# Kernel optimization log

Measured on AMD Instinct MI355X. Metric: run time of the kernel, lower is better.

Reference implementation:

```python
import jax, jax.numpy as jnp
import numpy as np

D_MODEL = 1280
NUM_EXPERTS = 20
HEAD_DIM = D_MODEL // NUM_EXPERTS  # 64
SCALE = HEAD_DIM ** -0.5


def setup_inputs() -> dict:
    key = jax.random.key(0)
    ks = jax.random.split(key, 8)
    B, S = 4, 1024
    s_in = 1.0 / np.sqrt(D_MODEL)
    x = jax.random.normal(ks[0], (B, S, D_MODEL), dtype=jnp.float32)
    # per-expert QKV projections stacked: [E, d_model, 3*head_dim]
    wqkv = jax.random.uniform(ks[1], (NUM_EXPERTS, D_MODEL, 3 * HEAD_DIM), jnp.float32, -s_in, s_in)
    bqkv = jax.random.uniform(ks[2], (NUM_EXPERTS, 3 * HEAD_DIM), jnp.float32, -s_in, s_in)
    router_w = jax.random.uniform(ks[3], (D_MODEL, NUM_EXPERTS), jnp.float32, -s_in, s_in)
    router_b = jax.random.uniform(ks[4], (NUM_EXPERTS,), jnp.float32, -s_in, s_in)
    out_w = jax.random.uniform(ks[5], (D_MODEL, D_MODEL), jnp.float32, -s_in, s_in)
    out_b = jax.random.uniform(ks[6], (D_MODEL,), jnp.float32, -s_in, s_in)
    return {"x": x, "wqkv": wqkv, "bqkv": bqkv, "router_w": router_w,
            "router_b": router_b, "out_w": out_w, "out_b": out_b}


def reference(x, wqkv, bqkv, router_w, router_b, out_w, out_b):
    # x: [B, S, D]
    B, S, D = x.shape
    E, H = NUM_EXPERTS, HEAD_DIM
    # router softmax gates (dropout = identity in eval)
    gates = jax.nn.softmax(x @ router_w + router_b, axis=-1)  # [B, S, E]
    # per-expert QKV: [E, B, S, 3H]
    qkv = jnp.einsum('bsd,edh->ebsh', x, wqkv) + bqkv[:, None, None, :]
    q, k, v = jnp.split(qkv, 3, axis=-1)  # each [E, B, S, H]
    scores = jnp.einsum('ebqh,ebkh->ebqk', q, k) * SCALE  # [E, B, S, S]
    attn = jax.nn.softmax(scores, axis=-1)
    eo = jnp.einsum('ebqk,ebkh->ebqh', attn, v)  # [E, B, S, H]
    # gate multiply and scatter into disjoint feature slices == concat over experts
    eo = eo * jnp.transpose(gates, (2, 0, 1))[..., None]  # [E, B, S, H]
    combined = jnp.transpose(eo, (1, 2, 0, 3)).reshape(B, S, E * H)  # [B, S, D]
    return combined @ out_w + out_b
```

## Files before the change

### kernel.cpp

```cpp
#include <hip/hip_runtime.h>
#include <hip/hip_bf16.h>

#define D_MODEL 1280
#define NUM_EXPERTS 20
#define HEAD_DIM 64
#define SEQ 1024
#define BATCH 4
#define BS_TOK 4096
#define QKV_N 192
#define QKV_W 3840

typedef __attribute__((ext_vector_type(8))) short short8;
typedef __attribute__((ext_vector_type(4))) float f32x4;
typedef __attribute__((ext_vector_type(16))) float f32x16;
typedef __hip_bfloat16 bf16;

static __device__ __forceinline__ void gload_lds16(const void* g, void* l) {
  __builtin_amdgcn_global_load_lds((const __attribute__((address_space(1))) void*)g,
                                   (__attribute__((address_space(3))) void*)l, 16, 0, 0);
}

__global__ __launch_bounds__(256) void k_rwT(const float* __restrict__ in,
                                             float* __restrict__ out) {
  int i = blockIdx.x * 256 + threadIdx.x;
  if (i < D_MODEL * NUM_EXPERTS) {
    int d = i / NUM_EXPERTS, e = i % NUM_EXPERTS;
    out[e * D_MODEL + d] = in[i];
  }
}

__global__ __launch_bounds__(256) void k_gates(const float* __restrict__ x,
    const float* __restrict__ rwT, const float* __restrict__ rb,
    float* __restrict__ gates, bf16* __restrict__ xb)
{
  __shared__ float xs[4][D_MODEL];
  __shared__ float logits[4][NUM_EXPERTS];
  const int r0 = blockIdx.x * 4;
  for (int i = threadIdx.x; i < 4 * (D_MODEL / 2); i += 256) {
    int r = i / (D_MODEL / 2), d2 = (i % (D_MODEL / 2)) * 2;
    float2 v = *(const float2*)(x + (size_t)(r0 + r) * D_MODEL + d2);
    xs[r][d2] = v.x; xs[r][d2 + 1] = v.y;
    __hip_bfloat162 h;
    h.x = __float2bfloat16(v.x); h.y = __float2bfloat16(v.y);
    *(__hip_bfloat162*)(xb + (size_t)(r0 + r) * D_MODEL + d2) = h;
  }
  __syncthreads();
  const int wid = threadIdx.x >> 6, lane = threadIdx.x & 63;
  for (int e = 0; e < NUM_EXPERTS; ++e) {
    float s = 0.f;
    #pragma unroll
    for (int j = 0; j < D_MODEL / 64; ++j) {
      int d = lane + 64 * j;
      s += xs[wid][d] * rwT[e * D_MODEL + d];
    }
    #pragma unroll
    for (int m = 32; m >= 1; m >>= 1) s += __shfl_xor(s, m);
    if (lane == 0) logits[wid][e] = s + rb[e];
  }
  __syncthreads();
  if (lane < 32) {
    float v = (lane < NUM_EXPERTS) ? logits[wid][lane] : -1e30f;
    float mx = v;
    #pragma unroll
    for (int m = 16; m >= 1; m >>= 1) mx = fmaxf(mx, __shfl_xor(mx, m, 32));
    float p = (lane < NUM_EXPERTS) ? __expf(v - mx) : 0.f;
    float sum = p;
    #pragma unroll
    for (int m = 16; m >= 1; m >>= 1) sum += __shfl_xor(sum, m, 32);
    if (lane < NUM_EXPERTS)
      gates[(size_t)(r0 + wid) * NUM_EXPERTS + lane] = p / sum;
  }
}

__global__ __launch_bounds__(256) void k_transpose(const float* __restrict__ in,
    bf16* __restrict__ out, int R, int C)
{
  __shared__ float tile[32][33];
  const size_t bo = (size_t)blockIdx.z * R * C;
  const int c0 = blockIdx.x * 32, r0 = blockIdx.y * 32;
  const int tx = threadIdx.x, ty = threadIdx.y;
  #pragma unroll
  for (int i = 0; i < 4; ++i)
    tile[ty + 8*i][tx] = in[bo + (size_t)(r0 + ty + 8*i) * C + (c0 + tx)];
  __syncthreads();
  #pragma unroll
  for (int i = 0; i < 4; ++i)
    out[bo + (size_t)(c0 + ty + 8*i) * R + (r0 + tx)] =
        __float2bfloat16(tile[tx][ty + 8*i]);
}

__global__ __launch_bounds__(512, 2) void k_gemm256(
    const bf16* __restrict__ A, const bf16* __restrict__ BT,
    const float* __restrict__ bias, bf16* __restrict__ C,
    int M, int N, int K)
{
  __shared__ __align__(16) bf16 lds[4][2][256 * 32];
  const int bid = blockIdx.x;
  const int xcd = bid & 7, c = bid >> 3;
  const int m0 = (xcd * 2 + (c & 1)) * 256;
  const int n0 = (c >> 1) * 256;
  const int tid = threadIdx.x, wid = tid >> 6, lane = tid & 63;
  const int wr = wid >> 2, wcn = wid & 3;
  const int fr = lane & 15, fg = lane >> 4;
  const int nt = K / 32;

  auto STAGE = [&](int t, int buf) {
    const bf16* Ag = A + (size_t)m0 * K + t * 32;
    const bf16* Bg = BT + (size_t)n0 * K + t * 32;
    #pragma unroll
    for (int i = 0; i < 2; ++i) {
      int idx = i * 512 + tid;
      int row = idx >> 2, sc = idx & 3;
      int g = sc ^ (row & 3);
      gload_lds16(Ag + (size_t)row * K + g * 8, &lds[buf][0][idx * 8]);
    }
    #pragma unroll
    for (int i = 0; i < 2; ++i) {
      int idx = i * 512 + tid;
      int row = idx >> 2, sc = idx & 3;
      int g = sc ^ (row & 3);
      gload_lds16(Bg + (size_t)row * K + g * 8, &lds[buf][1][idx * 8]);
    }
  };

  f32x4 acc[8][4] = {};
  auto COMPUTE = [&](int buf) {
    const bf16* As_ = &lds[buf][0][0];
    const bf16* Bs_ = &lds[buf][1][0];
    short8 af[8], bfv[4];
    #pragma unroll
    for (int mi = 0; mi < 8; ++mi) {
      int row = wr * 128 + mi * 16 + fr;
      int slot = fg ^ (row & 3);
      af[mi] = *(const short8*)(As_ + row * 32 + slot * 8);
    }
    #pragma unroll
    for (int ni = 0; ni < 4; ++ni) {
      int row = wcn * 64 + ni * 16 + fr;
      int slot = fg ^ (row & 3);
      bfv[ni] = *(const short8*)(Bs_ + row * 32 + slot * 8);
    }
    __builtin_amdgcn_s_setprio(1);
    #pragma unroll
    for (int mi = 0; mi < 8; ++mi) {
      #pragma unroll
      for (int ni = 0; ni < 4; ++ni)
        acc[mi][ni] = __builtin_amdgcn_mfma_f32_16x16x32_bf16(
            af[mi], bfv[ni], acc[mi][ni], 0, 0, 0);
    }
    __builtin_amdgcn_s_setprio(0);
  };

  STAGE(0, 0); STAGE(1, 1); STAGE(2, 2);
  asm volatile("s_waitcnt vmcnt(8)" ::: "memory");
  __builtin_amdgcn_s_barrier();
  __builtin_amdgcn_sched_barrier(0);
  int buf = 0;
  for (int t = 0; t < nt - 3; ++t) {
    int nb = buf + 3; nb = (nb >= 4) ? nb - 4 : nb;
    STAGE(t + 3, nb);
    COMPUTE(buf);
    asm volatile("s_waitcnt vmcnt(8)" ::: "memory");
    __builtin_amdgcn_s_barrier();
    __builtin_amdgcn_sched_barrier(0);
    buf = (buf == 3) ? 0 : buf + 1;
  }
  COMPUTE(buf);
  asm volatile("s_waitcnt vmcnt(4)" ::: "memory");
  __builtin_amdgcn_s_barrier();
  __builtin_amdgcn_sched_barrier(0);
  buf = (buf == 3) ? 0 : buf + 1;
  COMPUTE(buf);
  asm volatile("s_waitcnt vmcnt(0)" ::: "memory");
  __builtin_amdgcn_s_barrier();
  __builtin_amdgcn_sched_barrier(0);
  buf = (buf == 3) ? 0 : buf + 1;
  COMPUTE(buf);

  #pragma unroll
  for (int mi = 0; mi < 8; ++mi) {
    const int gr = m0 + wr * 128 + mi * 16 + fg * 4;
    #pragma unroll
    for (int ni = 0; ni < 4; ++ni) {
      const int gc = n0 + wcn * 64 + ni * 16 + fr;
      const float bv = bias[gc];
      #pragma unroll
      for (int r = 0; r < 4; ++r)
        C[(size_t)(gr + r) * N + gc] = __float2bfloat16(acc[mi][ni][r] + bv);
    }
  }
}

__global__ __launch_bounds__(512, 2) void k_gemm128r(
    const bf16* __restrict__ A, const bf16* __restrict__ BT,
    const float* __restrict__ bias, float* __restrict__ C,
    int M, int N, int K)
{
  __shared__ __align__(16) bf16 lds[4][2][128 * 32];
  const int bid = blockIdx.x;
  const int xcd = bid & 7, c = bid >> 3;
  const int m0 = (xcd * 4 + (c & 3)) * 128;
  const int n0 = (c >> 2) * 128;
  const int tid = threadIdx.x, wid = tid >> 6, lane = tid & 63;
  const int wr = wid >> 2, wcn = wid & 3;
  const int fr = lane & 15, fg = lane >> 4;
  const int nt = K / 32;

  auto STAGE = [&](int t, int buf) {
    const bf16* Ag = A + (size_t)m0 * K + t * 32;
    const bf16* Bg = BT + (size_t)n0 * K + t * 32;
    int row = tid >> 2, sc = tid & 3;
    int g = sc ^ (row & 3);
    gload_lds16(Ag + (size_t)row * K + g * 8, &lds[buf][0][tid * 8]);
    gload_lds16(Bg + (size_t)row * K + g * 8, &lds[buf][1][tid * 8]);
  };

  f32x4 acc[4][2] = {};
  auto COMPUTE = [&](int buf) {
    const bf16* As_ = &lds[buf][0][0];
    const bf16* Bs_ = &lds[buf][1][0];
    short8 af[4], bfv[2];
    #pragma unroll
    for (int mi = 0; mi < 4; ++mi) {
      int row = wr * 64 + mi * 16 + fr;
      int slot = fg ^ (row & 3);
      af[mi] = *(const short8*)(As_ + row * 32 + slot * 8);
    }
    #pragma unroll
    for (int ni = 0; ni < 2; ++ni) {
      int row = wcn * 32 + ni * 16 + fr;
      int slot = fg ^ (row & 3);
      bfv[ni] = *(const short8*)(Bs_ + row * 32 + slot * 8);
    }
    __builtin_amdgcn_s_setprio(1);
    #pragma unroll
    for (int mi = 0; mi < 4; ++mi) {
      #pragma unroll
      for (int ni = 0; ni < 2; ++ni)
        acc[mi][ni] = __builtin_amdgcn_mfma_f32_16x16x32_bf16(
            af[mi], bfv[ni], acc[mi][ni], 0, 0, 0);
    }
    __builtin_amdgcn_s_setprio(0);
  };

  STAGE(0, 0); STAGE(1, 1); STAGE(2, 2);
  asm volatile("s_waitcnt vmcnt(4)" ::: "memory");
  __builtin_amdgcn_s_barrier();
  __builtin_amdgcn_sched_barrier(0);
  int buf = 0;
  for (int t = 0; t < nt - 3; ++t) {
    int nb = buf + 3; nb = (nb >= 4) ? nb - 4 : nb;
    STAGE(t + 3, nb);
    COMPUTE(buf);
    asm volatile("s_waitcnt vmcnt(4)" ::: "memory");
    __builtin_amdgcn_s_barrier();
    __builtin_amdgcn_sched_barrier(0);
    buf = (buf == 3) ? 0 : buf + 1;
  }
  COMPUTE(buf);
  asm volatile("s_waitcnt vmcnt(2)" ::: "memory");
  __builtin_amdgcn_s_barrier();
  __builtin_amdgcn_sched_barrier(0);
  buf = (buf == 3) ? 0 : buf + 1;
  COMPUTE(buf);
  asm volatile("s_waitcnt vmcnt(0)" ::: "memory");
  __builtin_amdgcn_s_barrier();
  __builtin_amdgcn_sched_barrier(0);
  buf = (buf == 3) ? 0 : buf + 1;
  COMPUTE(buf);

  #pragma unroll
  for (int mi = 0; mi < 4; ++mi) {
    const int gr = m0 + wr * 64 + mi * 16 + fg * 4;
    #pragma unroll
    for (int ni = 0; ni < 2; ++ni) {
      const int gc = n0 + wcn * 32 + ni * 16 + fr;
      const float bv = bias[gc];
      #pragma unroll
      for (int r = 0; r < 4; ++r)
        C[(size_t)(gr + r) * N + gc] = acc[mi][ni][r] + bv;
    }
  }
}

__global__ __launch_bounds__(256, 4) void k_attn(
    const bf16* __restrict__ qkv, const float* __restrict__ gates,
    bf16* __restrict__ combined)
{
  __shared__ __align__(16) bf16 Ks[2][64 * 64];
  __shared__ __align__(16) bf16 VTs[64 * 64];
  __shared__ float Ltab[64];
  const int id = blockIdx.x;
  const int xcd = id & 7, kgrp = id >> 3;
  const int qt = kgrp / 10, bel = kgrp - qt * 10;
  const int be = xcd * 10 + bel;
  const int e = be >> 2, b = be & 3;
  const int s0 = qt * 64;
  const int tid = threadIdx.x, wid = tid >> 6, lane = tid & 63;
  const int l31 = lane & 31, hi = lane >> 5;
  const int qw = wid & 1, kh = wid >> 1;
  const bf16* base = qkv + (size_t)(b * SEQ) * QKV_W + e * QKV_N;
  const int rq = s0 + qw * 32 + l31;
  short8 qf[4];
  #pragma unroll
  for (int kc = 0; kc < 4; ++kc)
    qf[kc] = *(const short8*)(base + (size_t)rq * QKV_W + kc*16 + hi*8);
  f32x16 o0 = {}, o1 = {};
  float Lr = 0.f;
  const float CSC = 0.125f * 1.44269504f;

  const int kst_row = (lane >> 3);
  short8 vreg[2];
  auto KSTAGE = [&](int c0, int bsel) {
    #pragma unroll
    for (int p = 0; p < 2; ++p) {
      int W = p*4 + wid;
      int row = W*8 + kst_row;
      int g = (lane & 7) ^ W ^ kst_row;
      gload_lds16(base + (size_t)(c0 + row)*QKV_W + 64 + g*8,
                  &Ks[bsel][(W*64 + lane)*8]);
    }
  };
  auto VLOAD = [&](int c0) {
    #pragma unroll
    for (int it = 0; it < 2; ++it) {
      int key = it*32 + (tid >> 3);
      vreg[it] = *(const short8*)(base + (size_t)(c0 + key)*QKV_W + 128 + (tid & 7)*8);
    }
  };
  auto VWRITE = [&]() {
    #pragma unroll
    for (int it = 0; it < 2; ++it) {
      int key = it*32 + (tid >> 3);
      int h0b = tid & 7;
      int kc_ = key >> 3, ko = key & 7;
      union { short8 v; bf16 hh[8]; } u; u.v = vreg[it];
      #pragma unroll
      for (int j = 0; j < 8; ++j) {
        int scn = kc_ ^ h0b ^ j;
        VTs[(h0b*8 + j)*64 + scn*8 + ko] = u.hh[j];
      }
    }
  };

  KSTAGE(0, 0); VLOAD(0);
  int bsel = 0;
  const int krow = kh*32 + l31;
  const int Sk = ((krow >> 3) ^ krow) & 7;
  for (int t = 0; t < SEQ / 64; ++t) {
    if (t) __syncthreads();
    VWRITE();
    __syncthreads();
    if (t < SEQ / 64 - 1) { KSTAGE((t + 1) * 64, bsel ^ 1); VLOAD((t + 1) * 64); }
    f32x16 sc = {};
    __builtin_amdgcn_s_setprio(1);
    #pragma unroll
    for (int kc = 0; kc < 4; ++kc) {
      int st = (kc*2 + hi) ^ Sk;
      short8 kf = *(const short8*)(&Ks[bsel][krow*64 + st*8]);
      sc = __builtin_amdgcn_mfma_f32_32x32x16_bf16(kf, qf[kc], sc, 0, 0, 0);
    }
    __builtin_amdgcn_s_setprio(0);
    float p[16]; float ls = 0.f;
    #pragma unroll
    for (int i = 0; i < 16; ++i) { p[i] = exp2f(sc[i]*CSC); ls += p[i]; }
    Lr += ls + __shfl_xor(ls, 32);
    union { int w[4]; short8 v; } pf0, pf1;
    int ta, tb;
    asm("v_cvt_pk_bf16_f32 %0, %1, %2" : "=v"(ta) : "v"(p[0]), "v"(p[1]));
    asm("v_cvt_pk_bf16_f32 %0, %1, %2" : "=v"(tb) : "v"(p[4]), "v"(p[5]));
    asm volatile("v_permlane32_swap_b32 %0, %1" : "+v"(ta), "+v"(tb));
    pf0.w[0] = ta; pf0.w[2] = tb;
    asm("v_cvt_pk_bf16_f32 %0, %1, %2" : "=v"(ta) : "v"(p[2]), "v"(p[3]));
    asm("v_cvt_pk_bf16_f32 %0, %1, %2" : "=v"(tb) : "v"(p[6]), "v"(p[7]));
    asm volatile("v_permlane32_swap_b32 %0, %1" : "+v"(ta), "+v"(tb));
    pf0.w[1] = ta; pf0.w[3] = tb;
    asm("v_cvt_pk_bf16_f32 %0, %1, %2" : "=v"(ta) : "v"(p[8]), "v"(p[9]));
    asm("v_cvt_pk_bf16_f32 %0, %1, %2" : "=v"(tb) : "v"(p[12]), "v"(p[13]));
    asm volatile("v_permlane32_swap_b32 %0, %1" : "+v"(ta), "+v"(tb));
    pf1.w[0] = ta; pf1.w[2] = tb;
    asm("v_cvt_pk_bf16_f32 %0, %1, %2" : "=v"(ta) : "v"(p[10]), "v"(p[11]));
    asm("v_cvt_pk_bf16_f32 %0, %1, %2" : "=v"(tb) : "v"(p[14]), "v"(p[15]));
    asm volatile("v_permlane32_swap_b32 %0, %1" : "+v"(ta), "+v"(tb));
    pf1.w[1] = ta; pf1.w[3] = tb;
    __builtin_amdgcn_s_setprio(1);
    #pragma unroll
    for (int kb = 0; kb < 2; ++kb) {
      const short8 pv = (kb == 0) ? pf0.v : pf1.v;
      #pragma unroll
      for (int hb = 0; hb < 2; ++hb) {
        int h = hb*32 + l31;
        int cc = (kh*4 + kb*2 + hi) ^ (((h >> 3) ^ h) & 7);
        short8 vf = *(const short8*)(&VTs[h*64 + cc*8]);
        if (hb == 0) o0 = __builtin_amdgcn_mfma_f32_32x32x16_bf16(pv, vf, o0, 0, 0, 0);
        else         o1 = __builtin_amdgcn_mfma_f32_32x32x16_bf16(pv, vf, o1, 0, 0, 0);
      }
    }
    __builtin_amdgcn_s_setprio(0);
    bsel ^= 1;
  }
  __syncthreads();
  float* Ops = (float*)&Ks[0][0];
  float* Lp  = (float*)&VTs[0];
  if (kh == 1) {
    #pragma unroll
    for (int reg = 0; reg < 16; ++reg) {
      int crow = (reg & 3) + 8*(reg >> 2) + 4*hi;
      Ops[(qw*32 + crow)*64 + l31]      = o0[reg];
      Ops[(qw*32 + crow)*64 + 32 + l31] = o1[reg];
    }
    if (lane < 32) Lp[qw*32 + lane] = Lr;
  }
  __syncthreads();
  if (kh == 0) {
    #pragma unroll
    for (int reg = 0; reg < 16; ++reg) {
      int crow = (reg & 3) + 8*(reg >> 2) + 4*hi;
      o0[reg] += Ops[(qw*32 + crow)*64 + l31];
      o1[reg] += Ops[(qw*32 + crow)*64 + 32 + l31];
    }
    if (lane < 32) {
      float Lt = Lr + Lp[qw*32 + lane];
      float g = gates[(size_t)(b*SEQ + s0 + qw*32 + lane) * NUM_EXPERTS + e];
      Ltab[qw*32 + lane] = g / Lt;
    }
    const int rowbase = b*SEQ + s0 + qw*32;
    #pragma unroll
    for (int reg = 0; reg < 16; ++reg) {
      int crow = (reg & 3) + 8*(reg >> 2) + 4*hi;
      float inv = Ltab[qw*32 + crow];
      combined[(size_t)(rowbase + crow)*D_MODEL + e*64 + l31] =
          __float2bfloat16(o0[reg] * inv);
      combined[(size_t)(rowbase + crow)*D_MODEL + e*64 + 32 + l31] =
          __float2bfloat16(o1[reg] * inv);
    }
  }
}

extern "C" void kernel_launch(void* const* d_in, const int* in_sizes, int n_in,
                              void* d_out, int out_size, void* d_ws, size_t ws_size,
                              hipStream_t stream) {
  const float* x    = (const float*)d_in[0];
  const float* wqkv = (const float*)d_in[1];
  const float* bqkv = (const float*)d_in[2];
  const float* rw   = (const float*)d_in[3];
  const float* rb   = (const float*)d_in[4];
  const float* ow   = (const float*)d_in[5];
  const float* ob   = (const float*)d_in[6];
  char* ws = (char*)d_ws;
  bf16*  xb    = (bf16*)(ws);
  bf16*  wqkvT = (bf16*)(ws + 10485760);
  bf16*  owT   = (bf16*)(ws + 20316160);
  float* gates = (float*)(ws + 23592960);
  bf16*  qkv   = (bf16*)(ws + 23920640);
  bf16*  comb  = (bf16*)(ws + 55377920);
  float* rwT   = (float*)comb;

  k_rwT<<<(D_MODEL * NUM_EXPERTS + 255) / 256, 256, 0, stream>>>(rw, rwT);
  k_gates<<<1024, 256, 0, stream>>>(x, rwT, rb, gates, xb);
  k_transpose<<<dim3(6, 40, 20), dim3(32, 8), 0, stream>>>(wqkv, wqkvT, D_MODEL, QKV_N);
  k_transpose<<<dim3(40, 40, 1), dim3(32, 8), 0, stream>>>(ow, owT, D_MODEL, D_MODEL);
  k_gemm256<<<240, 512, 0, stream>>>(xb, wqkvT, bqkv, qkv, BS_TOK, QKV_W, D_MODEL);
  k_attn<<<1280, 256, 0, stream>>>(qkv, gates, comb);
  k_gemm128r<<<320, 512, 0, stream>>>(comb, owT, ob, (float*)d_out,
                                      BS_TOK, D_MODEL, D_MODEL);
}
```

Baseline: 156.2 us.

## Fold softmax scale into Q projection, defer row-sum reduction, tweak LDS swizzle

The QKV GEMM epilogue now multiplies Q columns by scale·log2(e), so the attention kernel can call exp2 on raw scores without a per-element multiply. Row sums are accumulated per register across all key tiles and reduced, including the cross-half shuffle, once after the loop instead of every iteration. Both GEMMs also change their LDS XOR swizzle to use (row>>1)&3, aiming to reduce bank conflicts on fragment reads. Rounding Q to bf16 after scaling changes numerics slightly, and the separate accumulator vector adds register pressure.

```diff
diff --git a/kernel.cpp b/kernel.cpp
--- a/kernel.cpp
+++ b/kernel.cpp
@@ -14,6 +14,8 @@
 typedef __attribute__((ext_vector_type(4))) float f32x4;
 typedef __attribute__((ext_vector_type(16))) float f32x16;
 typedef __hip_bfloat16 bf16;
+
+#define CSC_F 0.1803368801f
 
 static __device__ __forceinline__ void gload_lds16(const void* g, void* l) {
   __builtin_amdgcn_global_load_lds((const __attribute__((address_space(1))) void*)g,
@@ -111,14 +113,14 @@
     for (int i = 0; i < 2; ++i) {
       int idx = i * 512 + tid;
       int row = idx >> 2, sc = idx & 3;
-      int g = sc ^ (row & 3);
+      int g = sc ^ ((row >> 1) & 3);
       gload_lds16(Ag + (size_t)row * K + g * 8, &lds[buf][0][idx * 8]);
     }
     #pragma unroll
     for (int i = 0; i < 2; ++i) {
       int idx = i * 512 + tid;
       int row = idx >> 2, sc = idx & 3;
-      int g = sc ^ (row & 3);
+      int g = sc ^ ((row >> 1) & 3);
       gload_lds16(Bg + (size_t)row * K + g * 8, &lds[buf][1][idx * 8]);
     }
   };
@@ -131,13 +133,13 @@
     #pragma unroll
     for (int mi = 0; mi < 8; ++mi) {
       int row = wr * 128 + mi * 16 + fr;
-      int slot = fg ^ (row & 3);
+      int slot = fg ^ ((row >> 1) & 3);
       af[mi] = *(const short8*)(As_ + row * 32 + slot * 8);
     }
     #pragma unroll
     for (int ni = 0; ni < 4; ++ni) {
       int row = wcn * 64 + ni * 16 + fr;
-      int slot = fg ^ (row & 3);
+      int slot = fg ^ ((row >> 1) & 3);
       bfv[ni] = *(const short8*)(Bs_ + row * 32 + slot * 8);
     }
     __builtin_amdgcn_s_setprio(1);
@@ -184,9 +186,11 @@
     for (int ni = 0; ni < 4; ++ni) {
       const int gc = n0 + wcn * 64 + ni * 16 + fr;
       const float bv = bias[gc];
+      const bool isq = (gc % QKV_N) < 64;
+      const float sc_ = isq ? CSC_F : 1.0f;
       #pragma unroll
       for (int r = 0; r < 4; ++r)
-        C[(size_t)(gr + r) * N + gc] = __float2bfloat16(acc[mi][ni][r] + bv);
+        C[(size_t)(gr + r) * N + gc] = __float2bfloat16((acc[mi][ni][r] + bv) * sc_);
     }
   }
 }
@@ -210,7 +214,7 @@
     const bf16* Ag = A + (size_t)m0 * K + t * 32;
     const bf16* Bg = BT + (size_t)n0 * K + t * 32;
     int row = tid >> 2, sc = tid & 3;
-    int g = sc ^ (row & 3);
+    int g = sc ^ ((row >> 1) & 3);
     gload_lds16(Ag + (size_t)row * K + g * 8, &lds[buf][0][tid * 8]);
     gload_lds16(Bg + (size_t)row * K + g * 8, &lds[buf][1][tid * 8]);
   };
@@ -223,13 +227,13 @@
     #pragma unroll
     for (int mi = 0; mi < 4; ++mi) {
       int row = wr * 64 + mi * 16 + fr;
-      int slot = fg ^ (row & 3);
+      int slot = fg ^ ((row >> 1) & 3);
       af[mi] = *(const short8*)(As_ + row * 32 + slot * 8);
     }
     #pragma unroll
     for (int ni = 0; ni < 2; ++ni) {
       int row = wcn * 32 + ni * 16 + fr;
-      int slot = fg ^ (row & 3);
+      int slot = fg ^ ((row >> 1) & 3);
       bfv[ni] = *(const short8*)(Bs_ + row * 32 + slot * 8);
     }
     __builtin_amdgcn_s_setprio(1);
@@ -305,9 +309,7 @@
   #pragma unroll
   for (int kc = 0; kc < 4; ++kc)
     qf[kc] = *(const short8*)(base + (size_t)rq * QKV_W + kc*16 + hi*8);
-  f32x16 o0 = {}, o1 = {};
-  float Lr = 0.f;
-  const float CSC = 0.125f * 1.44269504f;
+  f32x16 o0 = {}, o1 = {}, Lacc = {};
 
   const int kst_row = (lane >> 3);
   short8 vreg[2];
@@ -361,10 +363,9 @@
       sc = __builtin_amdgcn_mfma_f32_32x32x16_bf16(kf, qf[kc], sc, 0, 0, 0);
     }
     __builtin_amdgcn_s_setprio(0);
-    float p[16]; float ls = 0.f;
-    #pragma unroll
-    for (int i = 0; i < 16; ++i) { p[i] = exp2f(sc[i]*CSC); ls += p[i]; }
-    Lr += ls + __shfl_xor(ls, 32);
+    float p[16];
+    #pragma unroll
+    for (int i = 0; i < 16; ++i) { p[i] = exp2f(sc[i]); Lacc[i] += p[i]; }
     union { int w[4]; short8 v; } pf0, pf1;
     int ta, tb;
     asm("v_cvt_pk_bf16_f32 %0, %1, %2" : "=v"(ta) : "v"(p[0]), "v"(p[1]));
@@ -399,6 +400,10 @@
     __builtin_amdgcn_s_setprio(0);
     bsel ^= 1;
   }
+  float Lr = 0.f;
+  #pragma unroll
+  for (int i = 0; i < 16; ++i) Lr += Lacc[i];
+  Lr += __shfl_xor(Lr, 32);
   __syncthreads();
   float* Ops = (float*)&Ks[0][0];
   float* Lp  = (float*)&VTs[0];
```

New measurement: 160.6 us. 2.9% more time.
